# Kernel optimization log

Hardware: AMD Instinct MI355X
Metric: run time of the kernel (lower is better)

Reference implementation:

```python
import math
import jax, jax.numpy as jnp
import numpy as np

B, S, D_MODEL, D_PROJ, N_ATTNS, NUM_CLASSES = 64, 300, 1024, 128, 4, 3862


def setup_inputs() -> dict:
    key = jax.random.key(0)
    ks = jax.random.split(key, 12)
    s = 1.0 / math.sqrt(D_MODEL)
    inp = {
        "seg_features": jax.random.normal(ks[0], (B, S, D_MODEL), dtype=jnp.float32),
        # per-head query linears (stacked): [H, d_proj, d_model]
        "Wq": jax.random.uniform(ks[1], (N_ATTNS, D_PROJ, D_MODEL), minval=-s, maxval=s, dtype=jnp.float32),
        "bq": jax.random.uniform(ks[2], (N_ATTNS, D_PROJ), minval=-s, maxval=s, dtype=jnp.float32),
        "Wk": jax.random.uniform(ks[3], (D_PROJ, D_MODEL), minval=-s, maxval=s, dtype=jnp.float32),
        "bk": jax.random.uniform(ks[4], (D_PROJ,), minval=-s, maxval=s, dtype=jnp.float32),
        "Wv": jax.random.uniform(ks[5], (D_PROJ, D_MODEL), minval=-s, maxval=s, dtype=jnp.float32),
        "bv": jax.random.uniform(ks[6], (D_PROJ,), minval=-s, maxval=s, dtype=jnp.float32),
        # conv1d(in=1, out=num_classes, kernel=d_proj) == linear [num_classes, d_proj]
        "Wc": jax.random.uniform(ks[7], (NUM_CLASSES, D_PROJ), minval=-1/math.sqrt(D_PROJ), maxval=1/math.sqrt(D_PROJ), dtype=jnp.float32),
        "bc": jax.random.uniform(ks[8], (NUM_CLASSES,), minval=-1/math.sqrt(D_PROJ), maxval=1/math.sqrt(D_PROJ), dtype=jnp.float32),
        "ln_a": jnp.ones((NUM_CLASSES,), dtype=jnp.float32),
        "ln_b": jnp.zeros((NUM_CLASSES,), dtype=jnp.float32),
    }
    return inp


def _layernorm(x, a, b, eps=1e-6):
    # torch LayerNorm variant: unbiased std, divide by (std + eps)
    mean = jnp.mean(x, axis=-1, keepdims=True)
    var = jnp.sum((x - mean) ** 2, axis=-1, keepdims=True) / (x.shape[-1] - 1)
    std = jnp.sqrt(var)
    return a * (x - mean) / (std + eps) + b


def reference(seg_features, Wq, bq, Wk, bk, Wv, bv, Wc, bc, ln_a, ln_b):
    scale = 1.0 / math.sqrt(D_PROJ)
    keys = jnp.einsum('bsd,pd->bsp', seg_features, Wk) + bk      # [B,S,P]
    vals = jnp.einsum('bsd,pd->bsp', seg_features, Wv) + bv      # [B,S,P]
    # all heads at once
    q = jnp.einsum('bsd,hpd->bhsp', seg_features, Wq) + bq[None, :, None, :]  # [B,H,S,P]
    score = jnp.einsum('bhsp,bsp->bhs', q, keys) * scale          # [B,H,S]
    p_attn = jax.nn.softmax(score, axis=-1)                       # [B,H,S]
    ws = jnp.einsum('bhs,bsp->bhp', p_attn, vals)                 # [B,H,P]
    logits = jnp.einsum('bhp,cp->bhc', jnp.maximum(ws, 0.0), Wc) + bc  # [B,H,C]
    logits = _layernorm(logits, ln_a, ln_b)                       # [B,H,C]
    logits = jnp.transpose(logits, (0, 2, 1))                     # [B,C,H]
    vid_logits = jnp.max(logits, axis=-1)                         # [B,C]
    attn_idc = jnp.argmax(logits, axis=-1)                        # [B,C]
    vid_probs = jax.nn.sigmoid(vid_logits)
    scores = jnp.transpose(score, (0, 2, 1))                      # [B,S,H]
    attn_weights = jnp.transpose(p_attn, (0, 2, 1))               # [B,S,H]
    # conv regularizer: conv applied to ones [B,1,P]
    conv_pars = jnp.sum(Wc, axis=-1)[None, :] + bc[None, :]       # [B? -> broadcast] -> [1,C]
    conv_pars = jnp.broadcast_to(conv_pars, (seg_features.shape[0], NUM_CLASSES))
    conv_pars = jax.nn.softmax(conv_pars, axis=1)
    mean_cp = jnp.mean(conv_pars, axis=1, keepdims=True)
    std_cp = jnp.sqrt(jnp.sum((conv_pars - mean_cp) ** 2, axis=1) / (NUM_CLASSES - 1))
    conv_loss = jnp.sum(jnp.clip(std_cp, 1e-9, 1e9), axis=0)
    return (vid_probs, attn_idc, scores, attn_weights, conv_loss)
```

## Files before the change

### kernel.cpp

```cpp
#include <hip/hip_runtime.h>
#include <math.h>

#define BATCH 64
#define SEQ 300
#define DM 1024
#define DP 128
#define NH 4
#define NC 3862
#define MROWS (BATCH*SEQ)
#define NSTK (6*DP)

#define BM 128
#define BN 64
#define BKK 16

__global__ __launch_bounds__(256) void proj_gemm(
    const float* __restrict__ X,
    const float* __restrict__ Wk, const float* __restrict__ bk,
    const float* __restrict__ Wv, const float* __restrict__ bv,
    const float* __restrict__ Wq, const float* __restrict__ bq,
    float* __restrict__ O)
{
    const int mtile = blockIdx.x;
    const int ntile = blockIdx.y;
    const int wsel  = ntile >> 1;
    const int nhalf = (ntile & 1) * BN;

    const float* Wbase; const float* bias;
    if (wsel == 0)      { Wbase = Wk; bias = bk; }
    else if (wsel == 1) { Wbase = Wv; bias = bv; }
    else                { Wbase = Wq + (size_t)(wsel - 2) * DP * DM;
                          bias  = bq + (wsel - 2) * DP; }
    Wbase += (size_t)nhalf * DM;
    bias  += nhalf;

    __shared__ double As[BKK][BM + 2];
    __shared__ double Bs[BKK][BN + 2];

    const int tid = threadIdx.x;
    const int tx = tid & 15, ty = tid >> 4;
    const int m0 = ty * 8, n0 = tx * 4;
    const int mbase = mtile * BM;

    const int lk = (tid & 3) * 4;
    const int lm = tid >> 2;

    double acc[8][4];
    #pragma unroll
    for (int i = 0; i < 8; ++i)
        #pragma unroll
        for (int j = 0; j < 4; ++j) acc[i][j] = 0.0;

    for (int k0 = 0; k0 < DM; k0 += BKK) {
        const float4 va0 = *reinterpret_cast<const float4*>(
            &X[(size_t)(mbase + lm) * DM + k0 + lk]);
        const float4 va1 = *reinterpret_cast<const float4*>(
            &X[(size_t)(mbase + lm + 64) * DM + k0 + lk]);
        const float4 vb = *reinterpret_cast<const float4*>(
            &Wbase[(size_t)lm * DM + k0 + lk]);

        As[lk + 0][lm] = (double)va0.x;
        As[lk + 1][lm] = (double)va0.y;
        As[lk + 2][lm] = (double)va0.z;
        As[lk + 3][lm] = (double)va0.w;
        As[lk + 0][lm + 64] = (double)va1.x;
        As[lk + 1][lm + 64] = (double)va1.y;
        As[lk + 2][lm + 64] = (double)va1.z;
        As[lk + 3][lm + 64] = (double)va1.w;
        Bs[lk + 0][lm] = (double)vb.x;
        Bs[lk + 1][lm] = (double)vb.y;
        Bs[lk + 2][lm] = (double)vb.z;
        Bs[lk + 3][lm] = (double)vb.w;
        __syncthreads();

        #pragma unroll
        for (int k = 0; k < BKK; ++k) {
            double a[8], b[4];
            #pragma unroll
            for (int i = 0; i < 8; ++i) a[i] = As[k][m0 + i];
            #pragma unroll
            for (int j = 0; j < 4; ++j) b[j] = Bs[k][n0 + j];
            #pragma unroll
            for (int i = 0; i < 8; ++i)
                #pragma unroll
                for (int j = 0; j < 4; ++j)
                    acc[i][j] = fma(a[i], b[j], acc[i][j]);
        }
        __syncthreads();
    }

    const double b0 = (double)bias[n0 + 0];
    const double b1 = (double)bias[n0 + 1];
    const double b2 = (double)bias[n0 + 2];
    const double b3 = (double)bias[n0 + 3];
    const int colbase = ntile * BN + n0;
    #pragma unroll
    for (int i = 0; i < 8; ++i) {
        float4 o;
        o.x = (float)(acc[i][0] + b0);
        o.y = (float)(acc[i][1] + b1);
        o.z = (float)(acc[i][2] + b2);
        o.w = (float)(acc[i][3] + b3);
        *reinterpret_cast<float4*>(
            &O[(size_t)(mbase + m0 + i) * NSTK + colbase]) = o;
    }
}

__global__ __launch_bounds__(256) void attn_kernel(
    const float* __restrict__ QKV,
    float* __restrict__ scores_out,
    float* __restrict__ attnw_out,
    double* __restrict__ wsrelu)
{
    const int b = blockIdx.x >> 2;
    const int h = blockIdx.x & 3;
    const int tid = threadIdx.x;
    const int wave = tid >> 6, lane = tid & 63;

    __shared__ double sc[SEQ];
    __shared__ double red[4];
    __shared__ double wacc[2][DP];

    const double scale = 0.08838834764831843;
    const float* base = QKV + (size_t)b * SEQ * NSTK;

    for (int s = wave; s < SEQ; s += 4) {
        const float* row = base + (size_t)s * NSTK;
        const float2 qv = *reinterpret_cast<const float2*>(row + 256 + h * DP + lane * 2);
        const float2 kv = *reinterpret_cast<const float2*>(row + lane * 2);
        double p = (double)qv.x * (double)kv.x + (double)qv.y * (double)kv.y;
        #pragma unroll
        for (int o = 32; o; o >>= 1) p += __shfl_xor(p, o);
        p *= scale;
        if (lane == 0) {
            sc[s] = p;
            scores_out[((size_t)b * SEQ + s) * NH + h] = (float)p;
        }
    }
    __syncthreads();

    double mx = -1e300;
    for (int i = tid; i < SEQ; i += 256) mx = fmax(mx, sc[i]);
    #pragma unroll
    for (int o = 32; o; o >>= 1) mx = fmax(mx, __shfl_xor(mx, o));
    if (lane == 0) red[wave] = mx;
    __syncthreads();
    mx = fmax(fmax(red[0], red[1]), fmax(red[2], red[3]));
    __syncthreads();

    double lsum = 0.0;
    for (int i = tid; i < SEQ; i += 256) {
        const double e = exp(sc[i] - mx);
        sc[i] = e;
        lsum += e;
    }
    #pragma unroll
    for (int o = 32; o; o >>= 1) lsum += __shfl_xor(lsum, o);
    if (lane == 0) red[wave] = lsum;
    __syncthreads();
    const double inv = 1.0 / (red[0] + red[1] + red[2] + red[3]);
    __syncthreads();
    for (int i = tid; i < SEQ; i += 256) {
        const double p = sc[i] * inv;
        sc[i] = p;
        attnw_out[((size_t)b * SEQ + i) * NH + h] = (float)p;
    }
    __syncthreads();

    const int p_idx = tid & 127, half = tid >> 7;
    double acc = 0.0;
    for (int s = half; s < SEQ; s += 2)
        acc = fma(sc[s], (double)base[(size_t)s * NSTK + 128 + p_idx], acc);
    wacc[half][p_idx] = acc;
    __syncthreads();
    if (tid < DP) {
        const double w = wacc[0][tid] + wacc[1][tid];
        wsrelu[((size_t)b * NH + h) * DP + tid] = fmax(w, 0.0);
    }
}

__global__ __launch_bounds__(256) void logits_kernel(
    const double* __restrict__ wsrelu, const float* __restrict__ Wc,
    const float* __restrict__ bc, double* __restrict__ logits,
    double* __restrict__ stats)
{
    const int bh = blockIdx.x;
    const int tid = threadIdx.x;
    const int wave = tid >> 6, lane = tid & 63;
    __shared__ double w4s[DP];
    __shared__ double red[4];
    if (tid < DP) w4s[tid] = wsrelu[(size_t)bh * DP + tid];
    __syncthreads();

    double lsum = 0.0;
    for (int c = tid; c < NC; c += 256) {
        const float4* wr = reinterpret_cast<const float4*>(Wc + (size_t)c * DP);
        double acc = 0.0;
        #pragma unroll
        for (int k = 0; k < 32; ++k) {
            const float4 v = wr[k];
            acc = fma((double)v.x, w4s[4 * k + 0], acc);
            acc = fma((double)v.y, w4s[4 * k + 1], acc);
            acc = fma((double)v.z, w4s[4 * k + 2], acc);
            acc = fma((double)v.w, w4s[4 * k + 3], acc);
        }
        acc += (double)bc[c];
        logits[(size_t)bh * NC + c] = acc;
        lsum += acc;
    }
    #pragma unroll
    for (int o = 32; o; o >>= 1) lsum += __shfl_xor(lsum, o);
    if (lane == 0) red[wave] = lsum;
    __syncthreads();
    const double mean = (red[0] + red[1] + red[2] + red[3]) / (double)NC;
    __syncthreads();

    double lss = 0.0;
    for (int c = tid; c < NC; c += 256) {
        const double d = logits[(size_t)bh * NC + c] - mean;
        lss = fma(d, d, lss);
    }
    #pragma unroll
    for (int o = 32; o; o >>= 1) lss += __shfl_xor(lss, o);
    if (lane == 0) red[wave] = lss;
    __syncthreads();
    if (tid == 0) {
        const double var = (red[0] + red[1] + red[2] + red[3]) / (double)(NC - 1);
        stats[bh * 2 + 0] = mean;
        stats[bh * 2 + 1] = sqrt(var);
    }
}

__global__ __launch_bounds__(256) void finalize_kernel(
    const double* __restrict__ logits, const double* __restrict__ stats,
    const float* __restrict__ ln_a, const float* __restrict__ ln_b,
    float* __restrict__ vid_probs, float* __restrict__ attn_idc)
{
    const int c = blockIdx.x * 256 + threadIdx.x;
    const int b = blockIdx.y;
    if (c >= NC) return;
    const double a = (double)ln_a[c], bb = (double)ln_b[c];
    double best = -1e300;
    int bi = 0;
    #pragma unroll
    for (int h = 0; h < NH; ++h) {
        const int bh = b * NH + h;
        const double x = logits[(size_t)bh * NC + c];
        const double ln = a * (x - stats[bh * 2]) / (stats[bh * 2 + 1] + 1e-6) + bb;
        if (ln > best) { best = ln; bi = h; }
    }
    vid_probs[(size_t)b * NC + c] = (float)(1.0 / (1.0 + exp(-best)));
    attn_idc[(size_t)b * NC + c] = (float)bi;
}

__global__ __launch_bounds__(256) void convloss_kernel(
    const float* __restrict__ Wc, const float* __restrict__ bc,
    float* __restrict__ out)
{
    __shared__ double t[NC];
    __shared__ double red[4];
    const int tid = threadIdx.x;
    const int wave = tid >> 6, lane = tid & 63;

    double lmax = -1e300;
    for (int c = tid; c < NC; c += 256) {
        const float4* wr = reinterpret_cast<const float4*>(Wc + (size_t)c * DP);
        double acc = 0.0;
        #pragma unroll
        for (int k = 0; k < 32; ++k) {
            const float4 v = wr[k];
            acc += (double)v.x + (double)v.y + (double)v.z + (double)v.w;
        }
        acc += (double)bc[c];
        t[c] = acc;
        lmax = fmax(lmax, acc);
    }
    #pragma unroll
    for (int o = 32; o; o >>= 1) lmax = fmax(lmax, __shfl_xor(lmax, o));
    if (lane == 0) red[wave] = lmax;
    __syncthreads();
    const double mx = fmax(fmax(red[0], red[1]), fmax(red[2], red[3]));
    __syncthreads();

    double lsum = 0.0;
    for (int c = tid; c < NC; c += 256) {
        const double e = exp(t[c] - mx);
        t[c] = e;
        lsum += e;
    }
    #pragma unroll
    for (int o = 32; o; o >>= 1) lsum += __shfl_xor(lsum, o);
    if (lane == 0) red[wave] = lsum;
    __syncthreads();
    const double inv = 1.0 / (red[0] + red[1] + red[2] + red[3]);
    __syncthreads();

    double psum = 0.0;
    for (int c = tid; c < NC; c += 256) {
        const double p = t[c] * inv;
        t[c] = p;
        psum += p;
    }
    #pragma unroll
    for (int o = 32; o; o >>= 1) psum += __shfl_xor(psum, o);
    if (lane == 0) red[wave] = psum;
    __syncthreads();
    const double mean = (red[0] + red[1] + red[2] + red[3]) / (double)NC;
    __syncthreads();

    double lss = 0.0;
    for (int c = tid; c < NC; c += 256) {
        const double d = t[c] - mean;
        lss = fma(d, d, lss);
    }
    #pragma unroll
    for (int o = 32; o; o >>= 1) lss += __shfl_xor(lss, o);
    if (lane == 0) red[wave] = lss;
    __syncthreads();
    if (tid == 0) {
        double stdv = sqrt((red[0] + red[1] + red[2] + red[3]) / (double)(NC - 1));
        stdv = fmin(fmax(stdv, 1e-9), 1e9);
        out[0] = (float)((double)BATCH * stdv);
    }
}

extern "C" void kernel_launch(void* const* d_in, const int* in_sizes, int n_in,
                              void* d_out, int out_size, void* d_ws, size_t ws_size,
                              hipStream_t stream)
{
    (void)in_sizes; (void)n_in; (void)out_size; (void)ws_size;
    const float* seg  = (const float*)d_in[0];
    const float* Wq   = (const float*)d_in[1];
    const float* bq   = (const float*)d_in[2];
    const float* Wk   = (const float*)d_in[3];
    const float* bk   = (const float*)d_in[4];
    const float* Wv   = (const float*)d_in[5];
    const float* bv   = (const float*)d_in[6];
    const float* Wc   = (const float*)d_in[7];
    const float* bc   = (const float*)d_in[8];
    const float* ln_a = (const float*)d_in[9];
    const float* ln_b = (const float*)d_in[10];

    float* out = (float*)d_out;
    float* vid_probs = out;
    float* attn_idc  = out + (size_t)BATCH * NC;
    float* scores    = attn_idc + (size_t)BATCH * NC;
    float* attnw     = scores + (size_t)BATCH * SEQ * NH;
    float* convl     = attnw + (size_t)BATCH * SEQ * NH;

    char* wsp = (char*)d_ws;
    float*  QKV    = (float*)wsp;
    wsp += (size_t)MROWS * NSTK * sizeof(float);
    double* wsrelu = (double*)wsp;
    wsp += (size_t)BATCH * NH * DP * sizeof(double);
    double* logits = (double*)wsp;
    wsp += (size_t)BATCH * NH * NC * sizeof(double);
    double* stats  = (double*)wsp;

    dim3 g1(MROWS / BM, NSTK / BN);
    proj_gemm<<<g1, 256, 0, stream>>>(seg, Wk, bk, Wv, bv, Wq, bq, QKV);

    attn_kernel<<<BATCH * NH, 256, 0, stream>>>(QKV, scores, attnw, wsrelu);

    logits_kernel<<<BATCH * NH, 256, 0, stream>>>(wsrelu, Wc, bc, logits, stats);

    dim3 g3((NC + 255) / 256, BATCH);
    finalize_kernel<<<g3, 256, 0, stream>>>(logits, stats, ln_a, ln_b, vid_probs, attn_idc);

    convloss_kernel<<<1, 256, 0, stream>>>(Wc, bc, convl);
}
```

Measured before the change: 994.3 us.

## Use FP64 MFMA with async global-to-LDS double-buffered loads in projection GEMM

```diff
diff --git a/kernel.cpp b/kernel.cpp
--- a/kernel.cpp
+++ b/kernel.cpp
@@ -11,10 +11,12 @@
 #define NSTK (6*DP)
 
 #define BM 128
-#define BN 64
-#define BKK 16
-
-__global__ __launch_bounds__(256) void proj_gemm(
+#define BN 128
+#define BK 16
+
+typedef double d4 __attribute__((ext_vector_type(4)));
+
+__global__ __launch_bounds__(256, 2) void proj_gemm_mfma(
     const float* __restrict__ X,
     const float* __restrict__ Wk, const float* __restrict__ bk,
     const float* __restrict__ Wv, const float* __restrict__ bv,
@@ -22,87 +24,97 @@
     float* __restrict__ O)
 {
     const int mtile = blockIdx.x;
-    const int ntile = blockIdx.y;
-    const int wsel  = ntile >> 1;
-    const int nhalf = (ntile & 1) * BN;
+    const int wsel  = blockIdx.y;
 
     const float* Wbase; const float* bias;
     if (wsel == 0)      { Wbase = Wk; bias = bk; }
     else if (wsel == 1) { Wbase = Wv; bias = bv; }
     else                { Wbase = Wq + (size_t)(wsel - 2) * DP * DM;
                           bias  = bq + (wsel - 2) * DP; }
-    Wbase += (size_t)nhalf * DM;
-    bias  += nhalf;
-
-    __shared__ double As[BKK][BM + 2];
-    __shared__ double Bs[BKK][BN + 2];
-
-    const int tid = threadIdx.x;
-    const int tx = tid & 15, ty = tid >> 4;
-    const int m0 = ty * 8, n0 = tx * 4;
+
+    __shared__ float As[2][BM * BK];
+    __shared__ float Bs[2][BN * BK];
+
+    const int tid  = threadIdx.x;
+    const int lane = tid & 63;
+    const int wave = tid >> 6;
+    const int wm = wave >> 1, wn = wave & 1;
     const int mbase = mtile * BM;
 
-    const int lk = (tid & 3) * 4;
-    const int lm = tid >> 2;
-
-    double acc[8][4];
-    #pragma unroll
-    for (int i = 0; i < 8; ++i)
-        #pragma unroll
-        for (int j = 0; j < 4; ++j) acc[i][j] = 0.0;
-
-    for (int k0 = 0; k0 < DM; k0 += BKK) {
-        const float4 va0 = *reinterpret_cast<const float4*>(
-            &X[(size_t)(mbase + lm) * DM + k0 + lk]);
-        const float4 va1 = *reinterpret_cast<const float4*>(
-            &X[(size_t)(mbase + lm + 64) * DM + k0 + lk]);
-        const float4 vb = *reinterpret_cast<const float4*>(
-            &Wbase[(size_t)lm * DM + k0 + lk]);
-
-        As[lk + 0][lm] = (double)va0.x;
-        As[lk + 1][lm] = (double)va0.y;
-        As[lk + 2][lm] = (double)va0.z;
-        As[lk + 3][lm] = (double)va0.w;
-        As[lk + 0][lm + 64] = (double)va1.x;
-        As[lk + 1][lm + 64] = (double)va1.y;
-        As[lk + 2][lm + 64] = (double)va1.z;
-        As[lk + 3][lm + 64] = (double)va1.w;
-        Bs[lk + 0][lm] = (double)vb.x;
-        Bs[lk + 1][lm] = (double)vb.y;
-        Bs[lk + 2][lm] = (double)vb.z;
-        Bs[lk + 3][lm] = (double)vb.w;
+    const int r = lane & 15;
+    const int g = lane >> 4;
+
+    d4 acc[4][4];
+    #pragma unroll
+    for (int mt = 0; mt < 4; ++mt)
+        #pragma unroll
+        for (int nt = 0; nt < 4; ++nt)
+            acc[mt][nt] = (d4)(0.0);
+
+#define STAGE(bufi, k0)                                                        \
+    do {                                                                       \
+        _Pragma("unroll")                                                      \
+        for (int j = 0; j < 2; ++j) {                                          \
+            const int slotbase = wave * 128 + j * 64;        \
+            const int slot = slotbase + lane;                                  \
+            const int mrow = slot >> 2;                                        \
+            const int kq4  = (slot & 3) << 2;                                  \
+            const float* srcA = &X[(size_t)(mbase + mrow) * DM + (k0) + kq4];  \
+            __builtin_amdgcn_global_load_lds(                                  \
+                (const __attribute__((address_space(1))) void*)srcA,           \
+                (__attribute__((address_space(3))) void*)&As[bufi][slotbase * 4], \
+                16, 0, 0);                                                     \
+            const float* srcB = &Wbase[(size_t)mrow * DM + (k0) + kq4];        \
+            __builtin_amdgcn_global_load_lds(                                  \
+                (const __attribute__((address_space(1))) void*)srcB,           \
+                (__attribute__((address_space(3))) void*)&Bs[bufi][slotbase * 4], \
+                16, 0, 0);                                                     \
+        }                                                                      \
+    } while (0)
+
+    STAGE(0, 0);
+    __syncthreads();
+
+    int buf = 0;
+    for (int t = 0; t < DM / BK; ++t) {
+        if (t + 1 < DM / BK) {
+            if (buf == 0) STAGE(1, (t + 1) * BK);
+            else          STAGE(0, (t + 1) * BK);
+        }
+        #pragma unroll
+        for (int kq = 0; kq < 4; ++kq) {
+            double a[4], b[4];
+            #pragma unroll
+            for (int mt = 0; mt < 4; ++mt)
+                a[mt] = (double)As[buf][(wm * 64 + mt * 16 + r) * BK + kq * 4 + g];
+            #pragma unroll
+            for (int nt = 0; nt < 4; ++nt)
+                b[nt] = (double)Bs[buf][(wn * 64 + nt * 16 + r) * BK + kq * 4 + g];
+            #pragma unroll
+            for (int mt = 0; mt < 4; ++mt)
+                #pragma unroll
+                for (int nt = 0; nt < 4; ++nt)
+                    acc[mt][nt] = __builtin_amdgcn_mfma_f64_16x16x4f64(
+                        a[mt], b[nt], acc[mt][nt], 0, 0, 0);
+        }
         __syncthreads();
-
-        #pragma unroll
-        for (int k = 0; k < BKK; ++k) {
-            double a[8], b[4];
+        buf ^= 1;
+    }
+#undef STAGE
+
+    #pragma unroll
+    for (int nt = 0; nt < 4; ++nt) {
+        const int col = wn * 64 + nt * 16 + r;
+        const double bi = (double)bias[col];
+        #pragma unroll
+        for (int mt = 0; mt < 4; ++mt) {
             #pragma unroll
-            for (int i = 0; i < 8; ++i) a[i] = As[k][m0 + i];
-            #pragma unroll
-            for (int j = 0; j < 4; ++j) b[j] = Bs[k][n0 + j];
-            #pragma unroll
-            for (int i = 0; i < 8; ++i)
-                #pragma unroll
-                for (int j = 0; j < 4; ++j)
-                    acc[i][j] = fma(a[i], b[j], acc[i][j]);
-        }
-        __syncthreads();
-    }
-
-    const double b0 = (double)bias[n0 + 0];
-    const double b1 = (double)bias[n0 + 1];
-    const double b2 = (double)bias[n0 + 2];
-    const double b3 = (double)bias[n0 + 3];
-    const int colbase = ntile * BN + n0;
-    #pragma unroll
-    for (int i = 0; i < 8; ++i) {
-        float4 o;
-        o.x = (float)(acc[i][0] + b0);
-        o.y = (float)(acc[i][1] + b1);
-        o.z = (float)(acc[i][2] + b2);
-        o.w = (float)(acc[i][3] + b3);
-        *reinterpret_cast<float4*>(
-            &O[(size_t)(mbase + m0 + i) * NSTK + colbase]) = o;
+            for (int i = 0; i < 4; ++i) {
+                const int row = wm * 64 + mt * 16 + g + 4 * i;
+                O[(size_t)(mbase + row) * NSTK + wsel * DP + col] =
+                    (float)(acc[mt][nt][i] + bi);
+            }
+        }
     }
 }
 
@@ -358,7 +370,7 @@
     double* stats  = (double*)wsp;
 
     dim3 g1(MROWS / BM, NSTK / BN);
-    proj_gemm<<<g1, 256, 0, stream>>>(seg, Wk, bk, Wv, bv, Wq, bq, QKV);
+    proj_gemm_mfma<<<g1, 256, 0, stream>>>(seg, Wk, bk, Wv, bv, Wq, bq, QKV);
 
     attn_kernel<<<BATCH * NH, 256, 0, stream>>>(QKV, scores, attnw, wsrelu);
 
```

Result: faster. 948.1 us (-4.6%).
